# Performance work log

Hardware: AMD Instinct MI355X
Metric: run time of the kernel (lower is better)

## Reference

```python
import jax, jax.numpy as jnp
import numpy as np

BITS = 4
GROUPSIZE = 128
MAXQ = 2 ** BITS - 1
PACK = 32 // BITS  # values packed per int32


def setup_inputs() -> dict:
    key = jax.random.key(0)
    k1, k2, k3, k4 = jax.random.split(key, 4)
    infeatures, outfeatures = 4096, 11008
    G = infeatures // GROUPSIZE  # 32 quantization groups
    x = jax.random.normal(k1, (16, 1, infeatures), dtype=jnp.float32)
    qweight = jax.random.randint(k2, (infeatures // PACK, outfeatures), 0, 2147483647, dtype=jnp.int32)
    scales = jax.random.uniform(k3, (G, outfeatures), dtype=jnp.float32)
    qzeros = jax.random.randint(k4, (G, outfeatures // PACK), 0, 2147483647, dtype=jnp.int32)
    return {"x": x, "qweight": qweight, "scales": scales, "qzeros": qzeros}


def _dequant(qweight, scales, qzeros):
    # shift amounts 0,4,8,...,28
    wf = jnp.arange(0, 32, BITS, dtype=jnp.int32)
    # unpack zero-points: [G, out/PACK, PACK] -> [G, 1, out]
    zeros = jnp.bitwise_and(jnp.right_shift(qzeros[:, :, None], wf[None, None, :]), MAXQ)
    zeros = zeros.reshape(zeros.shape[0], 1, -1).astype(scales.dtype)
    # unpack weights: [in/PACK, PACK, out] -> [G, GROUPSIZE, out]
    w = jnp.bitwise_and(jnp.right_shift(qweight[:, None, :], wf[None, :, None]), MAXQ)
    w = w.reshape(-1, GROUPSIZE, w.shape[-1]).astype(scales.dtype)
    sc = scales[:, None, :]  # [G, 1, out]
    weight = sc * w - sc * zeros  # per-group dequant
    return weight.reshape(-1, weight.shape[-1])  # [in, out]


def reference(x, qweight, scales, qzeros):
    W = _dequant(qweight, scales, qzeros)
    return jnp.matmul(x, W)  # [B, S, out]
```

## Files before the change

### kernel.cpp

```cpp
#include <hip/hip_runtime.h>


#define M_DIM 16
#define K_DIM 4096
#define N_DIM 11008
#define GS 128
#define KSPLIT 8
#define KC (K_DIM / KSPLIT)
#define GPC (KC / GS)
#define BLOCKN 64

typedef __attribute__((ext_vector_type(8))) short short8;
typedef __attribute__((ext_vector_type(4))) float f32x4;

__device__ __forceinline__ float bfl(unsigned w) {
    union { unsigned u; float f; } c; c.u = w << 16; return c.f;
}
__device__ __forceinline__ float bfh(unsigned w) {
    union { unsigned u; float f; } c; c.u = w & 0xFFFF0000u; return c.f;
}

__global__ __launch_bounds__(256) void qlin_fused(
    const float* __restrict__ x,
    const int*   __restrict__ qweight,
    const float* __restrict__ scales,
    const int*   __restrict__ qzeros,
    float*       __restrict__ outp,
    int nchunks)
{
    __shared__ __align__(16) unsigned short xs[M_DIM * KC];
    __shared__ __align__(16) float Xl[GPC * 16];

    const int tid  = threadIdx.x;
    const int lane = tid & 63, wave = tid >> 6;
    const int lmod = lane & 15, lhi = lane >> 4;
    const int n    = blockIdx.x * BLOCKN + wave * 16 + lmod;
    const int swzA = (lmod & 7) << 4;

    f32x4 outacc = {0.f, 0.f, 0.f, 0.f};

    for (int c = 0; c < nchunks; ++c) {
        const int ky0 = (blockIdx.y * nchunks + c) * KC;

        __syncthreads();
#pragma unroll
        for (int i = 0; i < (M_DIM * KC / 8) / 256; ++i) {
            const int idx = i * 256 + tid;
            const int m  = idx >> 6;
            const int cc = idx & 63;
            const float4* xp =
                (const float4*)(x + (size_t)m * K_DIM + ky0 + cc * 8);
            const float4 v0 = xp[0], v1 = xp[1];
            union { short8 s; unsigned u[4]; } pk;
            asm("v_cvt_pk_bf16_f32 %0, %1, %2" : "=v"(pk.u[0]) : "v"(v0.x), "v"(v1.x));
            asm("v_cvt_pk_bf16_f32 %0, %1, %2" : "=v"(pk.u[1]) : "v"(v0.y), "v"(v1.y));
            asm("v_cvt_pk_bf16_f32 %0, %1, %2" : "=v"(pk.u[2]) : "v"(v0.z), "v"(v1.z));
            asm("v_cvt_pk_bf16_f32 %0, %1, %2" : "=v"(pk.u[3]) : "v"(v0.w), "v"(v1.w));
            const int byte = ((m * KC + cc * 8) * 2) ^ ((m & 7) << 4);
            *(short8*)((char*)xs + byte) = pk.s;
        }
        __syncthreads();

        {
            const int g = wave;
            float xv = 0.f;
#pragma unroll
            for (int q = 0; q < 4; ++q) {
                const int byte =
                    ((lmod * KC + g * GS + lhi * 32 + q * 8) * 2) ^ swzA;
                union { short8 s; unsigned u[4]; } a;
                a.s = *(const short8*)((const char*)xs + byte);
#pragma unroll
                for (int p = 0; p < 4; ++p) xv += bfl(a.u[p]) + bfh(a.u[p]);
            }
            xv += __shfl_xor(xv, 16, 64);
            xv += __shfl_xor(xv, 32, 64);
            if (lane < 16) Xl[g * 16 + lane] = xv;
        }
        __syncthreads();

        const int rowbase = ky0 >> 3;
#pragma unroll
        for (int g = 0; g < GPC; ++g) {
            const int G = ky0 / GS + g;
            const float s = scales[G * N_DIM + n];
            const unsigned zq = (unsigned)qzeros[G * (N_DIM / 8) + (n >> 3)];
            const float z = (float)((zq >> ((n & 7) * 4)) & 15u);

            f32x4 acc = {0.f, 0.f, 0.f, 0.f};
#pragma unroll
            for (int t = 0; t < 4; ++t) {
                const unsigned qw = (unsigned)
                    qweight[(size_t)(rowbase + g * 16 + t * 4 + lhi) * N_DIM + n];
                union { short8 v; unsigned u[4]; } b;
                b.u[0] = ( qw        & 0x000F000Fu) | 0x43804380u;
                b.u[1] = ((qw >> 4)  & 0x000F000Fu) | 0x43804380u;
                b.u[2] = ((qw >> 8)  & 0x000F000Fu) | 0x43804380u;
                b.u[3] = ((qw >> 12) & 0x000F000Fu) | 0x43804380u;
                const int byte =
                    ((lmod * KC + g * GS + t * 32 + lhi * 8) * 2) ^ swzA;
                const short8 a = *(const short8*)((const char*)xs + byte);
                acc = __builtin_amdgcn_mfma_f32_16x16x32_bf16(a, b.v, acc, 0, 0, 0);
            }
            const f32x4 x4 = *(const f32x4*)&Xl[g * 16 + lhi * 4];
            const float s2 = 0.5f * s;
            const float zc = -s * (128.0f + z);
#pragma unroll
            for (int r = 0; r < 4; ++r)
                outacc[r] = fmaf(s2, acc[r], fmaf(zc, x4[r], outacc[r]));
        }
    }

#pragma unroll
    for (int r = 0; r < 4; ++r)
        outp[(size_t)(blockIdx.y * M_DIM + lhi * 4 + r) * N_DIM + n] = outacc[r];
}

__global__ __launch_bounds__(256) void qlin_reduce(
    const float* __restrict__ part, float* __restrict__ out)
{
    const int i = blockIdx.x * 256 + threadIdx.x;
    if (i < M_DIM * N_DIM) {
        float s = 0.f;
#pragma unroll
        for (int c = 0; c < KSPLIT; ++c)
            s += part[(size_t)c * M_DIM * N_DIM + i];
        out[i] = s;
    }
}

extern "C" void kernel_launch(void* const* d_in, const int* in_sizes, int n_in,
                              void* d_out, int out_size, void* d_ws, size_t ws_size,
                              hipStream_t stream) {
    const float* x       = (const float*)d_in[0];
    const int*   qweight = (const int*)d_in[1];
    const float* scales  = (const float*)d_in[2];
    const int*   qzeros  = (const int*)d_in[3];
    float*       out     = (float*)d_out;

    const size_t part_bytes = (size_t)KSPLIT * M_DIM * N_DIM * sizeof(float);
    if (ws_size >= part_bytes) {
        float* part = (float*)d_ws;
        dim3 grid(N_DIM / BLOCKN, KSPLIT);
        qlin_fused<<<grid, 256, 0, stream>>>(x, qweight, scales, qzeros, part, 1);
        qlin_reduce<<<(M_DIM * N_DIM + 255) / 256, 256, 0, stream>>>(part, out);
    } else {
        dim3 grid(N_DIM / BLOCKN, 1);
        qlin_fused<<<grid, 256, 0, stream>>>(x, qweight, scales, qzeros, out,
                                             KSPLIT);
    }
}
```

Baseline: 16.03 us.

## Hoist weight/scale/zero loads before x staging and widen blocks with deeper K-split

All qweight, scale and zero-point loads for a chunk are issued into registers before the x-to-bf16 staging and the barriers, so their global-memory latency overlaps the shared-memory setup instead of stalling each MFMA group. KSPLIT grows from 8 to 16 and blocks grow to 512 threads covering 128 columns, which halves the per-block x staging and raises the number of K-split blocks. The cost is more partial-sum traffic for the reduce kernel, which now reads 16 partial slices instead of 8, plus higher register pressure from holding the prefetched weights.

```diff
diff --git a/kernel.cpp b/kernel.cpp
--- a/kernel.cpp
+++ b/kernel.cpp
@@ -5,10 +5,11 @@
 #define K_DIM 4096
 #define N_DIM 11008
 #define GS 128
-#define KSPLIT 8
+#define KSPLIT 16
 #define KC (K_DIM / KSPLIT)
 #define GPC (KC / GS)
-#define BLOCKN 64
+#define BLOCKN 128
+#define NTHREADS 512
 
 typedef __attribute__((ext_vector_type(8))) short short8;
 typedef __attribute__((ext_vector_type(4))) float f32x4;
@@ -20,7 +21,7 @@
     union { unsigned u; float f; } c; c.u = w & 0xFFFF0000u; return c.f;
 }
 
-__global__ __launch_bounds__(256) void qlin_fused(
+__global__ __launch_bounds__(NTHREADS) void qlin_fused(
     const float* __restrict__ x,
     const int*   __restrict__ qweight,
     const float* __restrict__ scales,
@@ -41,13 +42,23 @@
 
     for (int c = 0; c < nchunks; ++c) {
         const int ky0 = (blockIdx.y * nchunks + c) * KC;
+        const int G0 = ky0 / GS, rowbase = ky0 >> 3;
+
+        float    sg[GPC]; unsigned zg[GPC]; unsigned qw[GPC][4];
+#pragma unroll
+        for (int g = 0; g < GPC; ++g) {
+            sg[g] = scales[(size_t)(G0 + g) * N_DIM + n];
+            zg[g] = (unsigned)qzeros[(size_t)(G0 + g) * (N_DIM / 8) + (n >> 3)];
+#pragma unroll
+            for (int t = 0; t < 4; ++t)
+                qw[g][t] = (unsigned)
+                    qweight[(size_t)(rowbase + g * 16 + t * 4 + lhi) * N_DIM + n];
+        }
 
         __syncthreads();
-#pragma unroll
-        for (int i = 0; i < (M_DIM * KC / 8) / 256; ++i) {
-            const int idx = i * 256 + tid;
-            const int m  = idx >> 6;
-            const int cc = idx & 63;
+        {
+            const int m  = tid >> 5;
+            const int cc = tid & 31;
             const float4* xp =
                 (const float4*)(x + (size_t)m * K_DIM + ky0 + cc * 8);
             const float4 v0 = xp[0], v1 = xp[1];
@@ -61,7 +72,7 @@
         }
         __syncthreads();
 
-        {
+        if (wave < GPC) {
             const int g = wave;
             float xv = 0.f;
 #pragma unroll
@@ -79,32 +90,26 @@
         }
         __syncthreads();
 
-        const int rowbase = ky0 >> 3;
 #pragma unroll
         for (int g = 0; g < GPC; ++g) {
-            const int G = ky0 / GS + g;
-            const float s = scales[G * N_DIM + n];
-            const unsigned zq = (unsigned)qzeros[G * (N_DIM / 8) + (n >> 3)];
-            const float z = (float)((zq >> ((n & 7) * 4)) & 15u);
-
             f32x4 acc = {0.f, 0.f, 0.f, 0.f};
 #pragma unroll
             for (int t = 0; t < 4; ++t) {
-                const unsigned qw = (unsigned)
-                    qweight[(size_t)(rowbase + g * 16 + t * 4 + lhi) * N_DIM + n];
                 union { short8 v; unsigned u[4]; } b;
-                b.u[0] = ( qw        & 0x000F000Fu) | 0x43804380u;
-                b.u[1] = ((qw >> 4)  & 0x000F000Fu) | 0x43804380u;
-                b.u[2] = ((qw >> 8)  & 0x000F000Fu) | 0x43804380u;
-                b.u[3] = ((qw >> 12) & 0x000F000Fu) | 0x43804380u;
+                const unsigned q = qw[g][t];
+                b.u[0] = ( q        & 0x000F000Fu) | 0x43804380u;
+                b.u[1] = ((q >> 4)  & 0x000F000Fu) | 0x43804380u;
+                b.u[2] = ((q >> 8)  & 0x000F000Fu) | 0x43804380u;
+                b.u[3] = ((q >> 12) & 0x000F000Fu) | 0x43804380u;
                 const int byte =
                     ((lmod * KC + g * GS + t * 32 + lhi * 8) * 2) ^ swzA;
                 const short8 a = *(const short8*)((const char*)xs + byte);
                 acc = __builtin_amdgcn_mfma_f32_16x16x32_bf16(a, b.v, acc, 0, 0, 0);
             }
             const f32x4 x4 = *(const f32x4*)&Xl[g * 16 + lhi * 4];
-            const float s2 = 0.5f * s;
-            const float zc = -s * (128.0f + z);
+            const float z  = (float)((zg[g] >> ((n & 7) * 4)) & 15u);
+            const float s2 = 0.5f * sg[g];
+            const float zc = -sg[g] * (128.0f + z);
 #pragma unroll
             for (int r = 0; r < 4; ++r)
                 outacc[r] = fmaf(s2, acc[r], fmaf(zc, x4[r], outacc[r]));
@@ -142,11 +147,12 @@
     if (ws_size >= part_bytes) {
         float* part = (float*)d_ws;
         dim3 grid(N_DIM / BLOCKN, KSPLIT);
-        qlin_fused<<<grid, 256, 0, stream>>>(x, qweight, scales, qzeros, part, 1);
+        qlin_fused<<<grid, NTHREADS, 0, stream>>>(x, qweight, scales, qzeros,
+                                                  part, 1);
         qlin_reduce<<<(M_DIM * N_DIM + 255) / 256, 256, 0, stream>>>(part, out);
     } else {
         dim3 grid(N_DIM / BLOCKN, 1);
-        qlin_fused<<<grid, 256, 0, stream>>>(x, qweight, scales, qzeros, out,
-                                             KSPLIT);
+        qlin_fused<<<grid, NTHREADS, 0, stream>>>(x, qweight, scales, qzeros,
+                                                  out, KSPLIT);
     }
 }
```

Result: slower. 17.47 us (+9.0%).
